# Kernel tuning notes

Hardware: AMD Instinct MI355X
Metric: run time of the kernel (lower is better)

## Reference

```python
import jax, jax.numpy as jnp
import numpy as np

NPOINTS = 4096


def farthest_point_sample(inp, npoints):
    """Iterative farthest point sampling.
    inp: [B, N, 3] float. Returns (out [B, npoints, 3], idx [B, npoints] int32).
    Matches the CUDA kernel semantics: first selected index is 0, running
    min-squared-distance buffer initialized to a large value (temp=1e10),
    each step picks the point farthest from the selected set.
    """
    B, N, _ = inp.shape
    init_idx = jnp.zeros((B,), dtype=jnp.int32)
    dist0 = jnp.full((B, N), 1e10, dtype=inp.dtype)

    def step(carry, _):
        dist, last_idx = carry
        # gather last selected point per batch: [B, 1, 3]
        last_pt = jnp.take_along_axis(inp, last_idx[:, None, None].astype(jnp.int32), axis=1)
        d = jnp.sum((inp - last_pt) ** 2, axis=-1)  # [B, N]
        dist = jnp.minimum(dist, d)
        nxt = jnp.argmax(dist, axis=-1).astype(jnp.int32)  # [B]
        return (dist, nxt), nxt

    (_, _), rest = jax.lax.scan(step, (dist0, init_idx), None, length=npoints - 1)
    idx = jnp.concatenate([init_idx[None, :], rest], axis=0).T  # [B, npoints]
    out = jnp.take_along_axis(inp, idx[..., None], axis=1)  # [B, npoints, 3]
    return out, idx


def setup_inputs() -> dict:
    key = jax.random.key(0)
    inp = jax.random.normal(key, (32, 131072, 3), dtype=jnp.float32)
    return {"inp": inp}


def reference(inp):
    return farthest_point_sample(inp, NPOINTS)
```

## Files before the change

### kernel.cpp

```cpp
#include <hip/hip_runtime.h>
#include <stdint.h>

#define NBATCH  32
#define NPTS    131072
#define NPOINTS 4096
#define BPB     8
#define TPB     512
#define PPT     32
#define PPB     (NPTS / BPB)

typedef unsigned long long u64;
typedef unsigned int u32;

#define SLOT_STRIDE 8


__global__ __attribute__((amdgpu_flat_work_group_size(TPB, TPB)))
void fps_kernel(const float* __restrict__ inp, float* __restrict__ out,
                u64* __restrict__ slots)
{
#pragma clang fp contract(off)
    extern __shared__ float2 XY[];

    const int bid  = blockIdx.x;
    const int b    = bid & 31;
    const int j    = bid >> 5;
    const int t    = threadIdx.x;
    const int lane = t & 63;
    const int wid  = t >> 6;

    const float* P  = inp + (size_t)b * NPTS * 3;
    float* outP     = out + (size_t)b * NPOINTS * 3;
    float* outIdx   = out + (size_t)NBATCH * NPOINTS * 3 + (size_t)b * NPOINTS;

    const int base = j * PPB;

    float pz[PPT], dist[PPT];
#pragma unroll
    for (int k = 0; k < PPT; ++k) {
        const int l = k * TPB + t;
        const float* pp = P + (size_t)(base + l) * 3;
        float x = pp[0], y = pp[1], z = pp[2];
        XY[l] = make_float2(x, y);
        pz[k] = z;
        asm volatile("" : "+v"(pz[k]));
        dist[k] = 1e10f;
    }

    float qx = P[0], qy = P[1], qz = P[2];

    if (j == 0 && t == 0) {
        outP[0] = qx; outP[1] = qy; outP[2] = qz;
        outIdx[0] = 0.0f;
    }

    u64* myslots = slots + (size_t)b * (2 * BPB * SLOT_STRIDE);

    __shared__ u64 skey[TPB / 64];
    __shared__ float sq[3];

    __syncthreads();

    for (int it = 0; it < NPOINTS - 1; ++it) {
        float m = -1.0f; int ki = 0;
#pragma unroll
        for (int k = 0; k < PPT; ++k) {
            float2 xy = XY[k * TPB + t];
            float dx = xy.x - qx;
            float dy = xy.y - qy;
            float dz = pz[k] - qz;
            float yy = dy * dy;
            asm("" : "+v"(yy));
            float d  = __builtin_fmaf(dz, dz,
                        __builtin_fmaf(dx, dx, yy));
            float nd = fminf(dist[k], d);
            dist[k] = nd;
            if (nd > m) { m = nd; ki = k; }
        }
        const int gi = base + ki * TPB + t;
        u64 key = ((u64)__float_as_uint(m) << 17) | (u64)(131071 - gi);

#pragma unroll
        for (int s = 1; s < 64; s <<= 1) {
            u64 o = __shfl_xor(key, s, 64);
            if (o > key) key = o;
        }
        if (lane == 0) skey[wid] = key;
        __syncthreads();

        if (wid == 0) {
            u64 k2 = (lane < TPB / 64) ? skey[lane] : 0ull;
#pragma unroll
            for (int s = 1; s < TPB / 64; s <<= 1) {
                u64 o = __shfl_xor(k2, s, 64);
                if (o > k2) k2 = o;
            }
            const int par = it & 1;
            const u64 tag = (u64)(it + 1) << 49;
            if (lane == 0) {
                __hip_atomic_store(&myslots[(par * BPB + j) * SLOT_STRIDE], tag | k2,
                                   __ATOMIC_RELEASE, __HIP_MEMORY_SCOPE_AGENT);
            }
            u64 v = 0;
            bool ok = (lane >= BPB);
            int guard = 0;
            while (true) {
                if (!ok) {
                    v = __hip_atomic_load(&myslots[(par * BPB + lane) * SLOT_STRIDE],
                                          __ATOMIC_ACQUIRE, __HIP_MEMORY_SCOPE_AGENT);
                    ok = (v >> 49) >= (u64)(it + 1);
                }
                if (__all((int)ok)) break;
                if (++guard > (1 << 20)) break;
            }
            u64 k3 = (lane < BPB) ? (v & ((1ull << 49) - 1)) : 0ull;
#pragma unroll
            for (int s = 1; s < BPB; s <<= 1) {
                u64 o = __shfl_xor(k3, s, 64);
                if (o > k3) k3 = o;
            }
            const int wgi = 131071 - (int)(k3 & 0x1FFFF);
            if (lane == 0) {
                const float* qp = P + (size_t)wgi * 3;
                float nqx = qp[0], nqy = qp[1], nqz = qp[2];
                sq[0] = nqx; sq[1] = nqy; sq[2] = nqz;
                if (j == 0) {
                    float* o3 = outP + (size_t)(it + 1) * 3;
                    o3[0] = nqx; o3[1] = nqy; o3[2] = nqz;
                    outIdx[it + 1] = (float)wgi;
                }
            }
        }
        __syncthreads();
        qx = sq[0]; qy = sq[1]; qz = sq[2];
    }
}

extern "C" void kernel_launch(void* const* d_in, const int* in_sizes, int n_in,
                              void* d_out, int out_size, void* d_ws, size_t ws_size,
                              hipStream_t stream)
{
    const float* inp = (const float*)d_in[0];
    float* outp      = (float*)d_out;
    u64* slots       = (u64*)d_ws;

    hipMemsetAsync(d_ws, 0,
                   (size_t)NBATCH * 2 * BPB * SLOT_STRIDE * sizeof(u64), stream);

    fps_kernel<<<NBATCH * BPB, TPB, (size_t)PPB * sizeof(float2), stream>>>(inp, outp, slots);
}
```

Baseline: 22.62 ms.

## Double blocks per batch and publish winner coordinates in sync slots

Raises the blocks per batch from 8 to 16, so each thread holds half as many points and the per-iteration scan gets shorter, at the cost of more blocks joining each cross-block handshake. Each block's leader now writes its local winner's coordinates next to the tagged key in the slot. After the barrier the final winner's coordinates come from the slots through wave shuffles, which takes the dependent global load of the winning point out of the critical path. Grid becomes 512 blocks of 512 threads, and every block of a batch must be resident at the same time for the spin barrier to finish.

```diff
diff --git a/kernel.cpp b/kernel.cpp
--- a/kernel.cpp
+++ b/kernel.cpp
@@ -4,9 +4,9 @@
 #define NBATCH  32
 #define NPTS    131072
 #define NPOINTS 4096
-#define BPB     8
+#define BPB     16
 #define TPB     512
-#define PPT     32
+#define PPT     16
 #define PPB     (NPTS / BPB)
 
 typedef unsigned long long u64;
@@ -43,12 +43,10 @@
         float x = pp[0], y = pp[1], z = pp[2];
         XY[l] = make_float2(x, y);
         pz[k] = z;
-        asm volatile("" : "+v"(pz[k]));
         dist[k] = 1e10f;
     }
 
     float qx = P[0], qy = P[1], qz = P[2];
-
     if (j == 0 && t == 0) {
         outP[0] = qx; outP[1] = qy; outP[2] = qz;
         outIdx[0] = 0.0f;
@@ -90,44 +88,64 @@
 
         if (wid == 0) {
             u64 k2 = (lane < TPB / 64) ? skey[lane] : 0ull;
+            u64 kk = k2;
 #pragma unroll
             for (int s = 1; s < TPB / 64; s <<= 1) {
-                u64 o = __shfl_xor(k2, s, 64);
-                if (o > k2) k2 = o;
+                u64 o = __shfl_xor(kk, s, 64);
+                if (o > kk) kk = o;
             }
             const int par = it & 1;
             const u64 tag = (u64)(it + 1) << 49;
             if (lane == 0) {
-                __hip_atomic_store(&myslots[(par * BPB + j) * SLOT_STRIDE], tag | k2,
+                const int bgi = 131071 - (int)(kk & 0x1FFFF);
+                const float* qp = P + (size_t)bgi * 3;
+                float wx = qp[0], wy = qp[1], wz = qp[2];
+                u64* slot = &myslots[(size_t)(par * BPB + j) * SLOT_STRIDE];
+                __hip_atomic_store(&slot[1],
+                                   ((u64)__float_as_uint(wy) << 32) | __float_as_uint(wx),
+                                   __ATOMIC_RELAXED, __HIP_MEMORY_SCOPE_AGENT);
+                __hip_atomic_store(&slot[2], (u64)__float_as_uint(wz),
+                                   __ATOMIC_RELAXED, __HIP_MEMORY_SCOPE_AGENT);
+                __hip_atomic_store(&slot[0], tag | kk,
                                    __ATOMIC_RELEASE, __HIP_MEMORY_SCOPE_AGENT);
             }
-            u64 v = 0;
+            u64 tw = 0;
             bool ok = (lane >= BPB);
             int guard = 0;
             while (true) {
                 if (!ok) {
-                    v = __hip_atomic_load(&myslots[(par * BPB + lane) * SLOT_STRIDE],
-                                          __ATOMIC_ACQUIRE, __HIP_MEMORY_SCOPE_AGENT);
-                    ok = (v >> 49) >= (u64)(it + 1);
+                    tw = __hip_atomic_load(&myslots[(size_t)(par * BPB + lane) * SLOT_STRIDE],
+                                           __ATOMIC_ACQUIRE, __HIP_MEMORY_SCOPE_AGENT);
+                    ok = (tw >> 49) >= (u64)(it + 1);
                 }
                 if (__all((int)ok)) break;
                 if (++guard > (1 << 20)) break;
             }
-            u64 k3 = (lane < BPB) ? (v & ((1ull << 49) - 1)) : 0ull;
+            u64 pxy = 0, pzz = 0, k3 = 0;
+            if (lane < BPB) {
+                u64* slot = &myslots[(size_t)(par * BPB + lane) * SLOT_STRIDE];
+                pxy = __hip_atomic_load(&slot[1], __ATOMIC_RELAXED, __HIP_MEMORY_SCOPE_AGENT);
+                pzz = __hip_atomic_load(&slot[2], __ATOMIC_RELAXED, __HIP_MEMORY_SCOPE_AGENT);
+                k3  = tw & ((1ull << 49) - 1);
+            }
+            u64 k3m = k3;
 #pragma unroll
             for (int s = 1; s < BPB; s <<= 1) {
-                u64 o = __shfl_xor(k3, s, 64);
-                if (o > k3) k3 = o;
+                u64 o = __shfl_xor(k3m, s, 64);
+                if (o > k3m) k3m = o;
             }
-            const int wgi = 131071 - (int)(k3 & 0x1FFFF);
+            int w3 = __ffsll(__ballot(k3 == k3m && lane < BPB)) - 1;
+            u64 wxy = __shfl(pxy, w3, 64);
+            u64 wzz = __shfl(pzz, w3, 64);
             if (lane == 0) {
-                const float* qp = P + (size_t)wgi * 3;
-                float nqx = qp[0], nqy = qp[1], nqz = qp[2];
+                float nqx = __uint_as_float((u32)wxy);
+                float nqy = __uint_as_float((u32)(wxy >> 32));
+                float nqz = __uint_as_float((u32)wzz);
                 sq[0] = nqx; sq[1] = nqy; sq[2] = nqz;
                 if (j == 0) {
                     float* o3 = outP + (size_t)(it + 1) * 3;
                     o3[0] = nqx; o3[1] = nqy; o3[2] = nqz;
-                    outIdx[it + 1] = (float)wgi;
+                    outIdx[it + 1] = (float)(131071 - (int)(k3m & 0x1FFFF));
                 }
             }
         }
```

After: 58.66 ms. 159% more time.
